# Kernel tuning notes

Measured on AMD Instinct MI355X. Metric: run time of the kernel, lower is better.

Reference implementation:

```python
import jax, jax.numpy as jnp
import numpy as np

L = 8        # num_layers
B = 4        # batch
S = 1024     # seq_len
D = 1024     # hidden_size
H = 16       # num_heads
FC = 4096    # fc_size
NEG = -1e9   # additive causal-mask value (matches torch code's -1000000000.0)


def setup_inputs() -> dict:
    key = jax.random.key(0)
    ks = jax.random.split(key, 12)
    std = 0.02
    inputs = jax.random.normal(ks[0], (B, S, D), jnp.float32)
    # per-layer stacked parameters; torch Linear y = x W^T + b, here stored as [in, out]
    Wq = jax.random.normal(ks[1], (L, D, D), jnp.float32) * std
    Wk = jax.random.normal(ks[2], (L, D, D), jnp.float32) * std
    Wv = jax.random.normal(ks[3], (L, D, D), jnp.float32) * std
    Wo = jax.random.normal(ks[4], (L, D, D), jnp.float32) * std
    W1 = jax.random.normal(ks[5], (L, D, FC), jnp.float32) * std
    W2 = jax.random.normal(ks[6], (L, FC, D), jnp.float32) * std
    bq = jnp.zeros((L, D), jnp.float32)
    bk = jnp.zeros((L, D), jnp.float32)
    bv = jnp.zeros((L, D), jnp.float32)
    bo = jnp.zeros((L, D), jnp.float32)
    b1 = jnp.zeros((L, FC), jnp.float32)
    b2 = jnp.zeros((L, D), jnp.float32)
    ln_g = jnp.ones((D,), jnp.float32)   # single LayerNorm shared across all sites
    ln_b = jnp.zeros((D,), jnp.float32)
    scale = jnp.asarray(0.1, jnp.float32)  # re-zero residual scale (init 0 in torch; 0.1 for non-degenerate test)
    return dict(inputs=inputs, Wq=Wq, bq=bq, Wk=Wk, bk=bk, Wv=Wv, bv=bv,
                Wo=Wo, bo=bo, W1=W1, b1=b1, W2=W2, b2=b2,
                ln_g=ln_g, ln_b=ln_b, scale=scale)


def reference(inputs, Wq, bq, Wk, bk, Wv, bv, Wo, bo, W1, b1, W2, b2, ln_g, ln_b, scale):
    Bz, Sl, Dm = inputs.shape
    nL = Wq.shape[0]
    dh = Dm // H
    inv_sqrt_dh = 1.0 / np.sqrt(dh).astype(np.float32)

    def layer_norm(x):  # shared gamma/beta, eps matches torch default 1e-5
        mu = jnp.mean(x, axis=-1, keepdims=True)
        var = jnp.var(x, axis=-1, keepdims=True)
        return (x - mu) * jax.lax.rsqrt(var + 1e-5) * ln_g + ln_b

    # causal additive bias [S, S], broadcasts over [B, H, S, S]
    bias = jnp.triu(jnp.full((Sl, Sl), NEG, inputs.dtype), k=1)

    x = inputs
    for i in range(nL):
        # --- masked self-attention block ---
        r = layer_norm(x)
        q = (r @ Wq[i] + bq[i]).reshape(Bz, Sl, H, dh)
        k = (r @ Wk[i] + bk[i]).reshape(Bz, Sl, H, dh)
        v = (r @ Wv[i] + bv[i]).reshape(Bz, Sl, H, dh)
        logits = jnp.einsum('bqhd,bkhd->bhqk', q, k) * inv_sqrt_dh + bias
        attn = jax.nn.softmax(logits, axis=-1)
        vals = jnp.einsum('bhqk,bkhd->bqhd', attn, v).reshape(Bz, Sl, Dm)
        r = vals @ Wo[i] + bo[i]
        x = x + scale * r  # re-zero residual (dropout is identity at inference)
        # --- FFN block ---
        r = layer_norm(x)
        r = jax.nn.gelu(r @ W1[i] + b1[i], approximate=False) @ W2[i] + b2[i]
        x = x + scale * r
    return layer_norm(x)
```

## Files before the change

### kernel.cpp

```cpp
#include <hip/hip_runtime.h>


typedef __bf16 bf16x8 __attribute__((ext_vector_type(8)));
typedef float  f32x4  __attribute__((ext_vector_type(4)));

#define DEV static __device__ __forceinline__

DEV unsigned short f2bf(float x) {
  unsigned u = __builtin_bit_cast(unsigned int, x);
  u += 0x7fffu + ((u >> 16) & 1u);
  return (unsigned short)(u >> 16);
}

DEV f32x4 mfma16(bf16x8 a, bf16x8 b, f32x4 c) {
  return __builtin_amdgcn_mfma_f32_16x16x32_bf16(a, b, c, 0, 0, 0);
}

DEV bf16x8 ldb8(const unsigned short* p) {
  return *reinterpret_cast<const bf16x8*>(p);
}

DEV void gload_lds16(const unsigned short* g, unsigned short* l) {
  __builtin_amdgcn_global_load_lds(
      (const __attribute__((address_space(1))) void*)g,
      (__attribute__((address_space(3))) void*)l, 16, 0, 0);
}

__global__ void transpose_cvt(const float* __restrict__ src,
                              unsigned short* __restrict__ dst,
                              int srcStride, int dstStride) {
  __shared__ float tile[32][33];
  const int t  = threadIdx.x;
  const int r  = t >> 3;
  const int c4 = (t & 7) << 2;
  const int k  = blockIdx.x * 32 + r;
  const int n0 = blockIdx.y * 32 + c4;
  const float4 v = *reinterpret_cast<const float4*>(src + (size_t)k * srcStride + n0);
  tile[r][c4] = v.x; tile[r][c4 + 1] = v.y; tile[r][c4 + 2] = v.z; tile[r][c4 + 3] = v.w;
  __syncthreads();
  const int n  = blockIdx.y * 32 + r;
  const int k0 = blockIdx.x * 32 + c4;
  ushort4 o;
  o.x = f2bf(tile[c4][r]);     o.y = f2bf(tile[c4 + 1][r]);
  o.z = f2bf(tile[c4 + 2][r]); o.w = f2bf(tile[c4 + 3][r]);
  *reinterpret_cast<ushort4*>(dst + (size_t)n * dstStride + k0) = o;
}

__global__ void transpose_cvt4(const float* __restrict__ Wq, const float* __restrict__ Wk,
                               const float* __restrict__ Wv, const float* __restrict__ Wo,
                               unsigned short* __restrict__ Wqkv_t,
                               unsigned short* __restrict__ Wo_t) {
  __shared__ float tile[32][33];
  const int z = blockIdx.z;
  const float* src = (z == 0) ? Wq : (z == 1) ? Wk : (z == 2) ? Wv : Wo;
  unsigned short* dst = (z == 3) ? Wo_t : (Wqkv_t + (size_t)z * 1024 * 1024);
  const int t  = threadIdx.x;
  const int r  = t >> 3;
  const int c4 = (t & 7) << 2;
  const int k  = blockIdx.x * 32 + r;
  const int n0 = blockIdx.y * 32 + c4;
  const float4 v = *reinterpret_cast<const float4*>(src + (size_t)k * 1024 + n0);
  tile[r][c4] = v.x; tile[r][c4 + 1] = v.y; tile[r][c4 + 2] = v.z; tile[r][c4 + 3] = v.w;
  __syncthreads();
  const int n  = blockIdx.y * 32 + r;
  const int k0 = blockIdx.x * 32 + c4;
  ushort4 o;
  o.x = f2bf(tile[c4][r]);     o.y = f2bf(tile[c4 + 1][r]);
  o.z = f2bf(tile[c4 + 2][r]); o.w = f2bf(tile[c4 + 3][r]);
  *reinterpret_cast<ushort4*>(dst + (size_t)n * 1024 + k0) = o;
}

__global__ void pack_qkv_bias(const float* __restrict__ bq, const float* __restrict__ bk,
                              const float* __restrict__ bv, float* __restrict__ out) {
  int i = blockIdx.x * 256 + threadIdx.x;
  out[i] = (i < 1024) ? bq[i] : (i < 2048 ? bk[i - 1024] : bv[i - 2048]);
}

template <int OUTF32>
__global__ void ln_kernel(const float* x, const float* __restrict__ gam,
                          const float* __restrict__ bet, void* out) {
  const int row = blockIdx.x;
  const int t   = threadIdx.x;
  const float* xr = x + (size_t)row * 1024;
  const float4 v = *reinterpret_cast<const float4*>(xr + t * 4);
  float s  = v.x + v.y + v.z + v.w;
  float ss = v.x * v.x + v.y * v.y + v.z * v.z + v.w * v.w;
  #pragma unroll
  for (int m = 32; m; m >>= 1) { s += __shfl_xor(s, m); ss += __shfl_xor(ss, m); }
  __shared__ float red[8];
  const int wv = t >> 6, ln = t & 63;
  if (ln == 0) { red[wv] = s; red[4 + wv] = ss; }
  __syncthreads();
  s  = red[0] + red[1] + red[2] + red[3];
  ss = red[4] + red[5] + red[6] + red[7];
  const float mean = s * (1.0f / 1024.0f);
  const float var  = ss * (1.0f / 1024.0f) - mean * mean;
  const float rstd = rsqrtf(var + 1e-5f);
  const float4 g  = *reinterpret_cast<const float4*>(gam + t * 4);
  const float4 bb = *reinterpret_cast<const float4*>(bet + t * 4);
  const float y0 = (v.x - mean) * rstd * g.x + bb.x;
  const float y1 = (v.y - mean) * rstd * g.y + bb.y;
  const float y2 = (v.z - mean) * rstd * g.z + bb.z;
  const float y3 = (v.w - mean) * rstd * g.w + bb.w;
  if (OUTF32) {
    float4 o; o.x = y0; o.y = y1; o.z = y2; o.w = y3;
    *reinterpret_cast<float4*>((float*)out + (size_t)row * 1024 + t * 4) = o;
  } else {
    ushort4 o; o.x = f2bf(y0); o.y = f2bf(y1); o.z = f2bf(y2); o.w = f2bf(y3);
    *reinterpret_cast<ushort4*>((unsigned short*)out + (size_t)row * 1024 + t * 4) = o;
  }
}

template <int MODE>
__global__ __launch_bounds__(512) void gemm8r(
    const unsigned short* __restrict__ A, const unsigned short* __restrict__ Bt,
    const float* __restrict__ bias, unsigned short* __restrict__ outb,
    unsigned short* __restrict__ vT, int N, int K) {
  __shared__ __attribute__((aligned(16))) unsigned short lds[7 * 8192];
  const int t = threadIdx.x, wave = t >> 6, lane = t & 63;
  const int wm = wave >> 2, wn = wave & 3;
  const int rl15 = lane & 15;

  const int nbn = N >> 8;
  const int qq  = gridDim.x >> 3;
  const int swz = (blockIdx.x & 7) * qq + (blockIdx.x >> 3);
  const int m0 = (swz / nbn) << 8, n0 = (swz % nbn) << 8;

  const unsigned short* aG = A  + (size_t)m0 * K;
  const unsigned short* bG = Bt + (size_t)n0 * K;

  const int srow = lane >> 2;
  const int ssl  = (((lane & 3) ^ ((srow >> 1) & 3)) << 3);
  const int swA  = (((lane >> 4) ^ ((lane >> 1) & 3)) << 3);

  auto stageA = [&](int slot, int kt) {
    #pragma unroll
    for (int j = 0; j < 2; ++j) {
      const int c = wave + j * 8;
      gload_lds16(aG + (size_t)(c * 16 + srow) * K + kt * 32 + ssl,
                  &lds[slot * 8192 + c * 512]);
    }
  };
  auto stageB = [&](int slot, int kt) {
    #pragma unroll
    for (int j = 0; j < 2; ++j) {
      const int c = wave + j * 8;
      gload_lds16(bG + (size_t)(c * 16 + srow) * K + kt * 32 + ssl,
                  &lds[slot * 8192 + c * 512]);
    }
  };

  const int nk = K >> 5;
  stageA(0, 0); stageB(1, 0);
  stageA(2, 1); stageB(3, 1);
  asm volatile("s_waitcnt vmcnt(4)" ::: "memory");
  asm volatile("s_barrier" ::: "memory");

  f32x4 acc[8][4] = {};
  int sA = 0, sB = 1, pA = 4, pB = 5;

  for (int kt = 0; kt < nk; ++kt) {
    const bool more = (kt + 2 < nk);
    if (more) { stageA(pA, kt + 2); stageB(pB, kt + 2); }
    const int ab = sA * 8192, bb = sB * 8192;
    bf16x8 af[8], bfr[4];
    #pragma unroll
    for (int mi = 0; mi < 8; ++mi)
      af[mi] = ldb8(&lds[ab + (wm * 128 + mi * 16 + rl15) * 32 + swA]);
    #pragma unroll
    for (int ni = 0; ni < 4; ++ni)
      bfr[ni] = ldb8(&lds[bb + (wn * 64 + ni * 16 + rl15) * 32 + swA]);
    __builtin_amdgcn_s_setprio(1);
    #pragma unroll
    for (int mi = 0; mi < 8; ++mi)
      #pragma unroll
      for (int ni = 0; ni < 4; ++ni)
        acc[mi][ni] = mfma16(af[mi], bfr[ni], acc[mi][ni]);
    __builtin_amdgcn_s_setprio(0);
    if (more) asm volatile("s_waitcnt vmcnt(4)" ::: "memory");
    else      asm volatile("s_waitcnt vmcnt(0)" ::: "memory");
    asm volatile("s_barrier" ::: "memory");
    sA += 2; if (sA >= 7) sA -= 7;
    sB += 2; if (sB >= 7) sB -= 7;
    pA += 2; if (pA >= 7) pA -= 7;
    pB += 2; if (pB >= 7) pB -= 7;
  }

  const int mrow = m0 + wm * 128 + (lane >> 4) * 4;
  const int ncol = n0 + wn * 64 + rl15;
  #pragma unroll
  for (int ni = 0; ni < 4; ++ni) {
    const int n = ncol + ni * 16;
    const float bn = bias[n];
    #pragma unroll
    for (int mi = 0; mi < 8; ++mi) {
      const int row0 = mrow + mi * 16;
      if constexpr (MODE == 3) {
        if (n >= 2048) {
          const int h = (n - 2048) >> 6, d = (n - 2048) & 63;
          const int b = row0 >> 10, s = row0 & 1023;
          ushort4 o;
          o.x = f2bf(acc[mi][ni][0] + bn); o.y = f2bf(acc[mi][ni][1] + bn);
          o.z = f2bf(acc[mi][ni][2] + bn); o.w = f2bf(acc[mi][ni][3] + bn);
          *reinterpret_cast<ushort4*>(vT + ((size_t)(b * 16 + h) * 64 + d) * 1024 + s) = o;
          continue;
        }
      }
      #pragma unroll
      for (int r = 0; r < 4; ++r) {
        const size_t idx = (size_t)(row0 + r) * N + n;
        float v = acc[mi][ni][r] + bn;
        if constexpr (MODE == 1)
          v = 0.5f * v * (1.0f + erff(v * 0.70710678118f));
        outb[idx] = f2bf(v);
      }
    }
  }
}

template <int MODE, int BN>
__global__ __launch_bounds__(256) void gemm2(
    const unsigned short* __restrict__ A, const unsigned short* __restrict__ Bt,
    const float* __restrict__ bias, unsigned short* __restrict__ outb,
    const float* xin, float* xout, const float* __restrict__ scale_p,
    unsigned short* __restrict__ vT, int N, int K) {
  constexpr int NI = BN / 32;
  constexpr int BSH = BN * 64;
  __shared__ __attribute__((aligned(16))) unsigned short lds[2][8192 + BSH];
  const int t = threadIdx.x, wave = t >> 6, lane = t & 63;
  const int m0 = blockIdx.x * 128, n0 = blockIdx.y * BN;
  const int wm = wave >> 1, wn = wave & 1;

  int srowA[4], scolA[4];
  #pragma unroll
  for (int j = 0; j < 4; ++j) {
    const int c = j * 256 + wave * 64 + lane;
    const int r = c >> 3;
    srowA[j] = r;
    scolA[j] = ((c & 7) ^ (r & 7)) << 3;
  }
  const unsigned short* aBase = A + (size_t)m0 * K;
  const unsigned short* bBase = Bt + (size_t)n0 * K;

  const int xk0 = (((lane >> 4)    ) ^ (lane & 7)) << 3;
  const int xk1 = (((lane >> 4) | 4) ^ (lane & 7)) << 3;
  const int arow = (wm * 64 + (lane & 15)) * 64;
  const int brow = (wn * (BN / 2) + (lane & 15)) * 64;

  f32x4 acc[4][NI] = {};
  const int nk = K >> 6;
  constexpr int BJ = NI;

  {
    unsigned short* l = &lds[0][0];
    #pragma unroll
    for (int j = 0; j < 4; ++j)
      gload_lds16(aBase + (size_t)srowA[j] * K + scolA[j], l + j * 2048 + wave * 512);
    #pragma unroll
    for (int j = 0; j < BJ; ++j)
      gload_lds16(bBase + (size_t)srowA[j] * K + scolA[j], l + 8192 + j * 2048 + wave * 512);
  }
  __syncthreads();

  int cur = 0;
  for (int kt = 0; kt < nk; ++kt) {
    if (kt + 1 < nk) {
      unsigned short* l = &lds[cur ^ 1][0];
      const int ko = (kt + 1) * 64;
      #pragma unroll
      for (int j = 0; j < 4; ++j)
        gload_lds16(aBase + (size_t)srowA[j] * K + ko + scolA[j], l + j * 2048 + wave * 512);
      #pragma unroll
      for (int j = 0; j < BJ; ++j)
        gload_lds16(bBase + (size_t)srowA[j] * K + ko + scolA[j], l + 8192 + j * 2048 + wave * 512);
    }
    const unsigned short* l = &lds[cur][0];
    #pragma unroll
    for (int kc = 0; kc < 2; ++kc) {
      const int xk = kc ? xk1 : xk0;
      bf16x8 a[4], b[NI];
      #pragma unroll
      for (int mi = 0; mi < 4; ++mi) a[mi] = ldb8(&l[arow + mi * 1024 + xk]);
      #pragma unroll
      for (int ni = 0; ni < NI; ++ni) b[ni] = ldb8(&l[8192 + brow + ni * 1024 + xk]);
      __builtin_amdgcn_s_setprio(1);
      #pragma unroll
      for (int mi = 0; mi < 4; ++mi)
        #pragma unroll
        for (int ni = 0; ni < NI; ++ni)
          acc[mi][ni] = mfma16(a[mi], b[ni], acc[mi][ni]);
      __builtin_amdgcn_s_setprio(0);
    }
    __syncthreads();
    cur ^= 1;
  }

  const int mrow = m0 + wm * 64 + (lane >> 4) * 4;
  const int ncol = n0 + wn * (BN / 2) + (lane & 15);
  float scl = 0.f;
  if constexpr (MODE == 2) scl = scale_p[0];
  #pragma unroll
  for (int ni = 0; ni < NI; ++ni) {
    const int n = ncol + ni * 16;
    const float bn = bias[n];
    #pragma unroll
    for (int mi = 0; mi < 4; ++mi) {
      const int row0 = mrow + mi * 16;
      if constexpr (MODE == 3) {
        if (n >= 2048) {
          const int h = (n - 2048) >> 6, d = (n - 2048) & 63;
          const int b = row0 >> 10, s = row0 & 1023;
          ushort4 o;
          o.x = f2bf(acc[mi][ni][0] + bn); o.y = f2bf(acc[mi][ni][1] + bn);
          o.z = f2bf(acc[mi][ni][2] + bn); o.w = f2bf(acc[mi][ni][3] + bn);
          *reinterpret_cast<ushort4*>(vT + ((size_t)(b * 16 + h) * 64 + d) * 1024 + s) = o;
          continue;
        }
      }
      #pragma unroll
      for (int r = 0; r < 4; ++r) {
        const size_t idx = (size_t)(row0 + r) * N + n;
        float v = acc[mi][ni][r] + bn;
        if constexpr (MODE == 1) {
          v = 0.5f * v * (1.0f + erff(v * 0.70710678118f));
          outb[idx] = f2bf(v);
        } else if constexpr (MODE == 2) {
          xout[idx] = xin[idx] + scl * v;
        } else {
          outb[idx] = f2bf(v);
        }
      }
    }
  }
}

__global__ __launch_bounds__(256) void attn_kernel(
    const unsigned short* __restrict__ qkv, const unsigned short* __restrict__ vT,
    unsigned short* __restrict__ vals) {
  const int bh = blockIdx.x & 63;
  const int g  = 15 - (blockIdx.x >> 6);
  const int b = bh >> 4, h = bh & 15;
  const int t = threadIdx.x, wave = t >> 6, lane = t & 63;
  const int rowLane = lane & 15, grp = lane >> 4;
  const int qt = g * 4 + wave;
  const int q0 = qt * 16;
  const int nkt = (qt >> 2) + 1;

  __shared__ __attribute__((aligned(16))) unsigned short P_lds[4][16 * 72];
  unsigned short* P = P_lds[wave];

  const unsigned short* qkvB  = qkv + (size_t)b * 1024 * 3072;
  const unsigned short* kBase = qkvB + 1024 + h * 64 + grp * 8;
  const unsigned short* vHead = vT + (size_t)bh * 64 * 1024;

  const unsigned short* qb = qkvB + (size_t)(q0 + rowLane) * 3072 + h * 64 + grp * 8;
  const bf16x8 aq0 = ldb8(qb);
  const bf16x8 aq1 = ldb8(qb + 32);

  f32x4 oacc[4] = {};
  float mrun[4], lrun[4];
  #pragma unroll
  for (int r = 0; r < 4; ++r) { mrun[r] = -1e30f; lrun[r] = 0.f; }

  bf16x8 k0[4], k1[4];
  #pragma unroll
  for (int nf = 0; nf < 4; ++nf) {
    const unsigned short* kb = kBase + (size_t)(nf * 16 + rowLane) * 3072;
    k0[nf] = ldb8(kb); k1[nf] = ldb8(kb + 32);
  }

  for (int kt = 0; kt < nkt; ++kt) {
    const int kv0 = kt * 64;
    bf16x8 v0[4], v1[4];
    #pragma unroll
    for (int df = 0; df < 4; ++df) {
      const unsigned short* vb = vHead + (size_t)(df * 16 + rowLane) * 1024 + kv0 + grp * 8;
      v0[df] = ldb8(vb); v1[df] = ldb8(vb + 32);
    }
    f32x4 sacc[4];
    #pragma unroll
    for (int nf = 0; nf < 4; ++nf) {
      f32x4 z = {0.f, 0.f, 0.f, 0.f};
      z = mfma16(aq0, k0[nf], z);
      z = mfma16(aq1, k1[nf], z);
      sacc[nf] = z;
    }
    if (kt + 1 < nkt) {
      #pragma unroll
      for (int nf = 0; nf < 4; ++nf) {
        const unsigned short* kb = kBase + (size_t)(kv0 + 64 + nf * 16 + rowLane) * 3072;
        k0[nf] = ldb8(kb); k1[nf] = ldb8(kb + 32);
      }
    }
    float pl[4][4], mx[4];
    #pragma unroll
    for (int r = 0; r < 4; ++r) {
      #pragma unroll
      for (int nf = 0; nf < 4; ++nf) pl[nf][r] = sacc[nf][r] * 0.125f;
    }
    if (kt == nkt - 1) {
      #pragma unroll
      for (int r = 0; r < 4; ++r) {
        const int qg = q0 + grp * 4 + r;
        #pragma unroll
        for (int nf = 0; nf < 4; ++nf)
          if (kv0 + nf * 16 + rowLane > qg) pl[nf][r] = -1e30f;
      }
    }
    #pragma unroll
    for (int r = 0; r < 4; ++r)
      mx[r] = fmaxf(fmaxf(pl[0][r], pl[1][r]), fmaxf(pl[2][r], pl[3][r]));
    #pragma unroll
    for (int m = 1; m <= 8; m <<= 1)
      #pragma unroll
      for (int r = 0; r < 4; ++r) mx[r] = fmaxf(mx[r], __shfl_xor(mx[r], m));
    float fac[4], rs[4];
    #pragma unroll
    for (int r = 0; r < 4; ++r) {
      const float mnew = fmaxf(mrun[r], mx[r]);
      fac[r] = __expf(mrun[r] - mnew);
      mrun[r] = mnew;
      float acc = 0.f;
      #pragma unroll
      for (int nf = 0; nf < 4; ++nf) {
        const float e = __expf(pl[nf][r] - mnew);
        pl[nf][r] = e;
        acc += e;
      }
      rs[r] = acc;
    }
    #pragma unroll
    for (int m = 1; m <= 8; m <<= 1)
      #pragma unroll
      for (int r = 0; r < 4; ++r) rs[r] += __shfl_xor(rs[r], m);
    #pragma unroll
    for (int r = 0; r < 4; ++r) lrun[r] = lrun[r] * fac[r] + rs[r];
    #pragma unroll
    for (int df = 0; df < 4; ++df)
      #pragma unroll
      for (int r = 0; r < 4; ++r) oacc[df][r] *= fac[r];
    #pragma unroll
    for (int nf = 0; nf < 4; ++nf)
      #pragma unroll
      for (int r = 0; r < 4; ++r)
        P[(grp * 4 + r) * 72 + nf * 16 + rowLane] = f2bf(pl[nf][r]);
    const bf16x8 pa0 = ldb8(&P[rowLane * 72 + grp * 8]);
    const bf16x8 pa1 = ldb8(&P[rowLane * 72 + 32 + grp * 8]);
    #pragma unroll
    for (int df = 0; df < 4; ++df) {
      oacc[df] = mfma16(pa0, v0[df], oacc[df]);
      oacc[df] = mfma16(pa1, v1[df], oacc[df]);
    }
  }
  float rl[4];
  #pragma unroll
  for (int r = 0; r < 4; ++r) rl[r] = 1.0f / lrun[r];
  #pragma unroll
  for (int df = 0; df < 4; ++df)
    #pragma unroll
    for (int r = 0; r < 4; ++r) {
      const int qg = q0 + grp * 4 + r;
      const float v = oacc[df][r] * rl[r];
      vals[(size_t)(b * 1024 + qg) * 1024 + h * 64 + df * 16 + rowLane] = f2bf(v);
    }
}

extern "C" void kernel_launch(void* const* d_in, const int* in_sizes, int n_in,
                              void* d_out, int out_size, void* d_ws, size_t ws_size,
                              hipStream_t stream) {
  (void)in_sizes; (void)n_in; (void)out_size; (void)ws_size;
  const float* inputs = (const float*)d_in[0];
  const float* Wq = (const float*)d_in[1];  const float* bq = (const float*)d_in[2];
  const float* Wk = (const float*)d_in[3];  const float* bk = (const float*)d_in[4];
  const float* Wv = (const float*)d_in[5];  const float* bv = (const float*)d_in[6];
  const float* Wo = (const float*)d_in[7];  const float* bo = (const float*)d_in[8];
  const float* W1 = (const float*)d_in[9];  const float* b1 = (const float*)d_in[10];
  const float* W2 = (const float*)d_in[11]; const float* b2 = (const float*)d_in[12];
  const float* ln_g = (const float*)d_in[13];
  const float* ln_b = (const float*)d_in[14];
  const float* scale_p = (const float*)d_in[15];
  float* xbuf = (float*)d_out;

  char* w = (char*)d_ws;
  size_t off = 0;
  auto take = [&](size_t bytes) {
    void* p = w + off;
    off = (off + bytes + 255) & ~(size_t)255;
    return p;
  };
  unsigned short* Wqkv_t = (unsigned short*)take((size_t)3072 * 1024 * 2);
  unsigned short* Wo_t   = (unsigned short*)take((size_t)1024 * 1024 * 2);
  unsigned short* W1_t   = (unsigned short*)take((size_t)4096 * 1024 * 2);
  unsigned short* W2_t   = (unsigned short*)take((size_t)1024 * 4096 * 2);
  float*          bqkv   = (float*)take(3072 * 4);
  unsigned short* rbuf   = (unsigned short*)take((size_t)4096 * 1024 * 2);
  unsigned short* qkvb   = (unsigned short*)take((size_t)4096 * 3072 * 2);
  unsigned short* vTb    = (unsigned short*)take((size_t)64 * 64 * 1024 * 2);
  unsigned short* valsb  = (unsigned short*)take((size_t)4096 * 1024 * 2);
  unsigned short* hbuf   = (unsigned short*)take((size_t)4096 * 4096 * 2);

  for (int i = 0; i < 8; ++i) {
    const float* xin = (i == 0) ? inputs : xbuf;
    transpose_cvt4<<<dim3(32, 32, 4), 256, 0, stream>>>(
        Wq + (size_t)i * 1024 * 1024, Wk + (size_t)i * 1024 * 1024,
        Wv + (size_t)i * 1024 * 1024, Wo + (size_t)i * 1024 * 1024, Wqkv_t, Wo_t);
    transpose_cvt<<<dim3(32, 128), 256, 0, stream>>>(W1 + (size_t)i * 1024 * 4096, W1_t, 4096, 1024);
    transpose_cvt<<<dim3(128, 32), 256, 0, stream>>>(W2 + (size_t)i * 4096 * 1024, W2_t, 1024, 4096);
    pack_qkv_bias<<<12, 256, 0, stream>>>(bq + i * 1024, bk + i * 1024, bv + i * 1024, bqkv);
    ln_kernel<0><<<4096, 256, 0, stream>>>(xin, ln_g, ln_b, rbuf);
    gemm8r<3><<<192, 512, 0, stream>>>(rbuf, Wqkv_t, bqkv, qkvb, vTb, 3072, 1024);
    attn_kernel<<<1024, 256, 0, stream>>>(qkvb, vTb, valsb);
    gemm2<2, 64><<<dim3(32, 16), 256, 0, stream>>>(valsb, Wo_t, bo + i * 1024, nullptr,
                                                   xin, xbuf, scale_p, nullptr, 1024, 1024);
    ln_kernel<0><<<4096, 256, 0, stream>>>(xbuf, ln_g, ln_b, rbuf);
    gemm8r<1><<<256, 512, 0, stream>>>(rbuf, W1_t, b1 + i * 4096, hbuf, nullptr, 4096, 1024);
    gemm2<2, 64><<<dim3(32, 16), 256, 0, stream>>>(hbuf, W2_t, b2 + i * 1024, nullptr,
                                                   xbuf, xbuf, scale_p, nullptr, 1024, 4096);
  }
  ln_kernel<1><<<4096, 256, 0, stream>>>(xbuf, ln_g, ln_b, xbuf);
}
```

Before: 2.104 ms.

## Use one wave per LayerNorm row and transpose attention score layout

LayerNorm now processes one row per wave, four rows per block. This drops the LDS reduction and the block barrier. The attention kernel swaps the MFMA operands so each lane holds scores for a single query row, which cuts the per-row max and sum reductions to two cross-lane shuffles instead of four rows times four shuffles. The rescale factors are then broadcast back with shuffles, the P tile write pattern changes, and the unused vT epilogue in gemm2 is removed. The layout change raises the risk of LDS bank conflicts on the P store.

```diff
diff --git a/kernel.cpp b/kernel.cpp
--- a/kernel.cpp
+++ b/kernel.cpp
@@ -77,37 +77,40 @@
 }
 
 template <int OUTF32>
-__global__ void ln_kernel(const float* x, const float* __restrict__ gam,
-                          const float* __restrict__ bet, void* out) {
-  const int row = blockIdx.x;
-  const int t   = threadIdx.x;
+__global__ __launch_bounds__(256) void ln_kernel(
+    const float* x, const float* __restrict__ gam,
+    const float* __restrict__ bet, void* out) {
+  const int t = threadIdx.x, wave = t >> 6, lane = t & 63;
+  const int row = blockIdx.x * 4 + wave;
   const float* xr = x + (size_t)row * 1024;
-  const float4 v = *reinterpret_cast<const float4*>(xr + t * 4);
-  float s  = v.x + v.y + v.z + v.w;
-  float ss = v.x * v.x + v.y * v.y + v.z * v.z + v.w * v.w;
-  #pragma unroll
-  for (int m = 32; m; m >>= 1) { s += __shfl_xor(s, m); ss += __shfl_xor(ss, m); }
-  __shared__ float red[8];
-  const int wv = t >> 6, ln = t & 63;
-  if (ln == 0) { red[wv] = s; red[4 + wv] = ss; }
-  __syncthreads();
-  s  = red[0] + red[1] + red[2] + red[3];
-  ss = red[4] + red[5] + red[6] + red[7];
+  float4 v[4];
+  float s = 0.f, ss = 0.f;
+  #pragma unroll
+  for (int k = 0; k < 4; ++k) {
+    v[k] = *reinterpret_cast<const float4*>(xr + k * 256 + lane * 4);
+    s  += v[k].x + v[k].y + v[k].z + v[k].w;
+    ss += v[k].x * v[k].x + v[k].y * v[k].y + v[k].z * v[k].z + v[k].w * v[k].w;
+  }
+  #pragma unroll
+  for (int m = 1; m <= 32; m <<= 1) { s += __shfl_xor(s, m); ss += __shfl_xor(ss, m); }
   const float mean = s * (1.0f / 1024.0f);
   const float var  = ss * (1.0f / 1024.0f) - mean * mean;
   const float rstd = rsqrtf(var + 1e-5f);
-  const float4 g  = *reinterpret_cast<const float4*>(gam + t * 4);
-  const float4 bb = *reinterpret_cast<const float4*>(bet + t * 4);
-  const float y0 = (v.x - mean) * rstd * g.x + bb.x;
-  const float y1 = (v.y - mean) * rstd * g.y + bb.y;
-  const float y2 = (v.z - mean) * rstd * g.z + bb.z;
-  const float y3 = (v.w - mean) * rstd * g.w + bb.w;
-  if (OUTF32) {
-    float4 o; o.x = y0; o.y = y1; o.z = y2; o.w = y3;
-    *reinterpret_cast<float4*>((float*)out + (size_t)row * 1024 + t * 4) = o;
-  } else {
-    ushort4 o; o.x = f2bf(y0); o.y = f2bf(y1); o.z = f2bf(y2); o.w = f2bf(y3);
-    *reinterpret_cast<ushort4*>((unsigned short*)out + (size_t)row * 1024 + t * 4) = o;
+  #pragma unroll
+  for (int k = 0; k < 4; ++k) {
+    const float4 g  = *reinterpret_cast<const float4*>(gam + k * 256 + lane * 4);
+    const float4 bb = *reinterpret_cast<const float4*>(bet + k * 256 + lane * 4);
+    const float y0 = (v[k].x - mean) * rstd * g.x + bb.x;
+    const float y1 = (v[k].y - mean) * rstd * g.y + bb.y;
+    const float y2 = (v[k].z - mean) * rstd * g.z + bb.z;
+    const float y3 = (v[k].w - mean) * rstd * g.w + bb.w;
+    if (OUTF32) {
+      float4 o; o.x = y0; o.y = y1; o.z = y2; o.w = y3;
+      *reinterpret_cast<float4*>((float*)out + (size_t)row * 1024 + k * 256 + lane * 4) = o;
+    } else {
+      ushort4 o; o.x = f2bf(y0); o.y = f2bf(y1); o.z = f2bf(y2); o.w = f2bf(y3);
+      *reinterpret_cast<ushort4*>((unsigned short*)out + (size_t)row * 1024 + k * 256 + lane * 4) = o;
+    }
   }
 }
 
@@ -223,7 +226,7 @@
     const unsigned short* __restrict__ A, const unsigned short* __restrict__ Bt,
     const float* __restrict__ bias, unsigned short* __restrict__ outb,
     const float* xin, float* xout, const float* __restrict__ scale_p,
-    unsigned short* __restrict__ vT, int N, int K) {
+    int N, int K) {
   constexpr int NI = BN / 32;
   constexpr int BSH = BN * 64;
   __shared__ __attribute__((aligned(16))) unsigned short lds[2][8192 + BSH];
@@ -305,21 +308,9 @@
     const float bn = bias[n];
     #pragma unroll
     for (int mi = 0; mi < 4; ++mi) {
-      const int row0 = mrow + mi * 16;
-      if constexpr (MODE == 3) {
-        if (n >= 2048) {
-          const int h = (n - 2048) >> 6, d = (n - 2048) & 63;
-          const int b = row0 >> 10, s = row0 & 1023;
-          ushort4 o;
-          o.x = f2bf(acc[mi][ni][0] + bn); o.y = f2bf(acc[mi][ni][1] + bn);
-          o.z = f2bf(acc[mi][ni][2] + bn); o.w = f2bf(acc[mi][ni][3] + bn);
-          *reinterpret_cast<ushort4*>(vT + ((size_t)(b * 16 + h) * 64 + d) * 1024 + s) = o;
-          continue;
-        }
-      }
       #pragma unroll
       for (int r = 0; r < 4; ++r) {
-        const size_t idx = (size_t)(row0 + r) * N + n;
+        const size_t idx = (size_t)(mrow + mi * 16 + r) * N + n;
         float v = acc[mi][ni][r] + bn;
         if constexpr (MODE == 1) {
           v = 0.5f * v * (1.0f + erff(v * 0.70710678118f));
@@ -358,9 +349,7 @@
   const bf16x8 aq1 = ldb8(qb + 32);
 
   f32x4 oacc[4] = {};
-  float mrun[4], lrun[4];
-  #pragma unroll
-  for (int r = 0; r < 4; ++r) { mrun[r] = -1e30f; lrun[r] = 0.f; }
+  float mrun = -1e30f, lrun = 0.f;
 
   bf16x8 k0[4], k1[4];
   #pragma unroll
@@ -381,8 +370,8 @@
     #pragma unroll
     for (int nf = 0; nf < 4; ++nf) {
       f32x4 z = {0.f, 0.f, 0.f, 0.f};
-      z = mfma16(aq0, k0[nf], z);
-      z = mfma16(aq1, k1[nf], z);
+      z = mfma16(k0[nf], aq0, z);
+      z = mfma16(k1[nf], aq1, z);
       sacc[nf] = z;
     }
     if (kt + 1 < nkt) {
@@ -392,58 +381,53 @@
         k0[nf] = ldb8(kb); k1[nf] = ldb8(kb + 32);
       }
     }
-    float pl[4][4], mx[4];
-    #pragma unroll
-    for (int r = 0; r < 4; ++r) {
-      #pragma unroll
-      for (int nf = 0; nf < 4; ++nf) pl[nf][r] = sacc[nf][r] * 0.125f;
-    }
+    float pl[4][4];
+    #pragma unroll
+    for (int nf = 0; nf < 4; ++nf)
+      #pragma unroll
+      for (int r = 0; r < 4; ++r) pl[nf][r] = sacc[nf][r] * 0.125f;
     if (kt == nkt - 1) {
+      const int qg = q0 + rowLane;
+      #pragma unroll
+      for (int nf = 0; nf < 4; ++nf)
+        #pragma unroll
+        for (int r = 0; r < 4; ++r)
+          if (kv0 + nf * 16 + grp * 4 + r > qg) pl[nf][r] = -1e30f;
+    }
+    float mloc = pl[0][0];
+    #pragma unroll
+    for (int nf = 0; nf < 4; ++nf)
+      #pragma unroll
+      for (int r = 0; r < 4; ++r) mloc = fmaxf(mloc, pl[nf][r]);
+    mloc = fmaxf(mloc, __shfl_xor(mloc, 16));
+    mloc = fmaxf(mloc, __shfl_xor(mloc, 32));
+    const float mnew = fmaxf(mrun, mloc);
+    const float facq = __expf(mrun - mnew);
+    mrun = mnew;
+    float sloc = 0.f;
+    #pragma unroll
+    for (int nf = 0; nf < 4; ++nf)
       #pragma unroll
       for (int r = 0; r < 4; ++r) {
-        const int qg = q0 + grp * 4 + r;
-        #pragma unroll
-        for (int nf = 0; nf < 4; ++nf)
-          if (kv0 + nf * 16 + rowLane > qg) pl[nf][r] = -1e30f;
-      }
-    }
-    #pragma unroll
-    for (int r = 0; r < 4; ++r)
-      mx[r] = fmaxf(fmaxf(pl[0][r], pl[1][r]), fmaxf(pl[2][r], pl[3][r]));
-    #pragma unroll
-    for (int m = 1; m <= 8; m <<= 1)
-      #pragma unroll
-      for (int r = 0; r < 4; ++r) mx[r] = fmaxf(mx[r], __shfl_xor(mx[r], m));
-    float fac[4], rs[4];
-    #pragma unroll
-    for (int r = 0; r < 4; ++r) {
-      const float mnew = fmaxf(mrun[r], mx[r]);
-      fac[r] = __expf(mrun[r] - mnew);
-      mrun[r] = mnew;
-      float acc = 0.f;
-      #pragma unroll
-      for (int nf = 0; nf < 4; ++nf) {
         const float e = __expf(pl[nf][r] - mnew);
         pl[nf][r] = e;
-        acc += e;
+        sloc += e;
       }
-      rs[r] = acc;
-    }
-    #pragma unroll
-    for (int m = 1; m <= 8; m <<= 1)
-      #pragma unroll
-      for (int r = 0; r < 4; ++r) rs[r] += __shfl_xor(rs[r], m);
-    #pragma unroll
-    for (int r = 0; r < 4; ++r) lrun[r] = lrun[r] * fac[r] + rs[r];
+    sloc += __shfl_xor(sloc, 16);
+    sloc += __shfl_xor(sloc, 32);
+    lrun = lrun * facq + sloc;
+    float fac_r[4];
+    #pragma unroll
+    for (int r = 0; r < 4; ++r) fac_r[r] = __shfl(facq, grp * 4 + r);
     #pragma unroll
     for (int df = 0; df < 4; ++df)
       #pragma unroll
-      for (int r = 0; r < 4; ++r) oacc[df][r] *= fac[r];
+      for (int r = 0; r < 4; ++r) oacc[df][r] *= fac_r[r];
     #pragma unroll
     for (int nf = 0; nf < 4; ++nf)
       #pragma unroll
       for (int r = 0; r < 4; ++r)
-        P[(grp * 4 + r) * 72 + nf * 16 + rowLane] = f2bf(pl[nf][r]);
+        P[rowLane * 72 + nf * 16 + grp * 4 + r] = f2bf(pl[nf][r]);
     const bf16x8 pa0 = ldb8(&P[rowLane * 72 + grp * 8]);
     const bf16x8 pa1 = ldb8(&P[rowLane * 72 + 32 + grp * 8]);
     #pragma unroll
@@ -452,9 +436,10 @@
       oacc[df] = mfma16(pa1, v1[df], oacc[df]);
     }
   }
+  const float rlq = 1.0f / lrun;
   float rl[4];
   #pragma unroll
-  for (int r = 0; r < 4; ++r) rl[r] = 1.0f / lrun[r];
+  for (int r = 0; r < 4; ++r) rl[r] = __shfl(rlq, grp * 4 + r);
   #pragma unroll
   for (int df = 0; df < 4; ++df)
     #pragma unroll
@@ -507,15 +492,15 @@
     transpose_cvt<<<dim3(32, 128), 256, 0, stream>>>(W1 + (size_t)i * 1024 * 4096, W1_t, 4096, 1024);
     transpose_cvt<<<dim3(128, 32), 256, 0, stream>>>(W2 + (size_t)i * 4096 * 1024, W2_t, 1024, 4096);
     pack_qkv_bias<<<12, 256, 0, stream>>>(bq + i * 1024, bk + i * 1024, bv + i * 1024, bqkv);
-    ln_kernel<0><<<4096, 256, 0, stream>>>(xin, ln_g, ln_b, rbuf);
+    ln_kernel<0><<<1024, 256, 0, stream>>>(xin, ln_g, ln_b, rbuf);
     gemm8r<3><<<192, 512, 0, stream>>>(rbuf, Wqkv_t, bqkv, qkvb, vTb, 3072, 1024);
     attn_kernel<<<1024, 256, 0, stream>>>(qkvb, vTb, valsb);
     gemm2<2, 64><<<dim3(32, 16), 256, 0, stream>>>(valsb, Wo_t, bo + i * 1024, nullptr,
-                                                   xin, xbuf, scale_p, nullptr, 1024, 1024);
-    ln_kernel<0><<<4096, 256, 0, stream>>>(xbuf, ln_g, ln_b, rbuf);
+                                                   xin, xbuf, scale_p, 1024, 1024);
+    ln_kernel<0><<<1024, 256, 0, stream>>>(xbuf, ln_g, ln_b, rbuf);
     gemm8r<1><<<256, 512, 0, stream>>>(rbuf, W1_t, b1 + i * 4096, hbuf, nullptr, 4096, 1024);
     gemm2<2, 64><<<dim3(32, 16), 256, 0, stream>>>(hbuf, W2_t, b2 + i * 1024, nullptr,
-                                                   xbuf, xbuf, scale_p, nullptr, 1024, 4096);
-  }
-  ln_kernel<1><<<4096, 256, 0, stream>>>(xbuf, ln_g, ln_b, xbuf);
-}
+                                                   xbuf, xbuf, scale_p, 1024, 4096);
+  }
+  ln_kernel<1><<<1024, 256, 0, stream>>>(xbuf, ln_g, ln_b, xbuf);
+}
```

New measurement: 2.087 ms. About the same (-0.8%).
